# Kernel optimization log

Measured on AMD Instinct MI355X. Metric: run time of the kernel, lower is better.

## Reference

```python
import jax, jax.numpy as jnp
import numpy as np

NUM_ELEM = 62
DEGREE = 3
M = 64  # matrix_size = sqrt(layer_sizes[0]) = sqrt(4096)
IN_DIM, H = 4096, 2048
N_POINTS = 2_097_152


def _glorot(k, shape):
    lim = np.float32(np.sqrt(2.0 / (shape[0] + shape[1])))
    return jax.random.normal(k, shape, jnp.float32) * lim


def setup_inputs() -> dict:
    key = jax.random.key(0)
    ks = jax.random.split(key, 4)
    points = jax.random.uniform(ks[0], (N_POINTS, 2), jnp.float32)
    # first coordinate lives in [-1, 1) (original maps it via (x+1)/2)
    points = points.at[:, 0].set(points[:, 0] * 2.0 - 1.0)
    return {
        "points": points,
        "W1": _glorot(ks[1], (IN_DIM, H)), "b1": jnp.zeros((H,), jnp.float32),
        "W2": _glorot(ks[2], (H, H)),      "b2": jnp.zeros((H,), jnp.float32),
        "W3": _glorot(ks[3], (H, 1)),      "b3": jnp.zeros((1,), jnp.float32),
    }


def _quadratic(t):
    # tfg bspline._quadratic: 3 quadratic B-spline basis functions of t in [0,1)
    return jnp.stack([(1.0 - t) ** 2 * 0.5, -t * t + t + 0.5, t * t * 0.5], axis=-1)


def _spline(coord):
    p = coord * NUM_ELEM
    pos = jnp.minimum(jnp.floor(p).astype(jnp.int32) + 1, NUM_ELEM)  # tf.cond clamp
    return _quadratic(jnp.mod(p, 1.0)), pos


def reference(points, W1, b1, W2, b2, W3, b3):
    # cofs = eye(4096); identity @ W1 == W1, so the first Dense reduces to W1 + b1
    h = jnp.tanh(W1 + b1)
    h = jnp.tanh(h @ W2 + b2)
    out = jnp.tanh(h @ W3 + b3)          # [4096, 1]
    u = out.reshape(M, M) * 3.0           # control-point grid [64, 64]

    x = (points[:, 0] + 1.0) * 0.5
    y = points[:, 1]
    bx, px = _spline(x)                   # bx: [N,3], px: [N]
    by, py = _spline(y)
    offs = jnp.arange(DEGREE)
    ix = px[:, None] - 1 + offs           # [N,3] row indices into u
    iy = py[:, None] - 1 + offs           # [N,3] col indices into u
    Wn = u[ix[:, :, None], iy[:, None, :]]  # [N,3,3] local control-point windows
    # sum_{i,j} W[i,j] * splines_x[i] * splines_y[j]  (meshgrid orientation)
    return jnp.einsum('nij,ni,nj->n', Wn, bx, by)
```

## Files before the change

### kernel.cpp

```cpp
#include <hip/hip_runtime.h>
#include <stdint.h>

#define IN_DIM 4096
#define H_DIM  2048
#define NPTS   2097152

typedef short  bf16x8  __attribute__((ext_vector_type(8)));
typedef float  floatx4 __attribute__((ext_vector_type(4)));

__device__ __forceinline__ unsigned short f2bf(float f) {
    unsigned u = __float_as_uint(f);
    unsigned r = (u + 0x7FFFu + ((u >> 16) & 1u)) >> 16;
    return (unsigned short)r;
}

__global__ void prep_h(const float* __restrict__ W1, const float* __restrict__ b1,
                       unsigned short* __restrict__ hbf, float* __restrict__ rowsum) {
    if (blockIdx.x < 16) rowsum[blockIdx.x * 256 + threadIdx.x] = 0.0f;
    int idx = (blockIdx.x * 256 + threadIdx.x) * 4;
    float4 w = *(const float4*)(W1 + idx);
    float4 b = *(const float4*)(b1 + (idx & (H_DIM - 1)));
    ushort4 o;
    o.x = f2bf(tanhf(w.x + b.x));
    o.y = f2bf(tanhf(w.y + b.y));
    o.z = f2bf(tanhf(w.z + b.z));
    o.w = f2bf(tanhf(w.w + b.w));
    *(ushort4*)(hbf + idx) = o;
}

__global__ void prep_w2t(const float* __restrict__ W2, unsigned short* __restrict__ W2T) {
    __shared__ unsigned short tile[64][66];
    int k0 = blockIdx.y * 64, n0 = blockIdx.x * 64;
    for (int idx = threadIdx.x; idx < 64 * 64; idx += 256) {
        int r = idx >> 6, c = idx & 63;
        tile[c][r] = f2bf(W2[(size_t)(k0 + r) * H_DIM + n0 + c]);
    }
    __syncthreads();
    for (int idx = threadIdx.x; idx < 64 * 64; idx += 256) {
        int r = idx >> 6, c = idx & 63;
        W2T[(size_t)(n0 + r) * H_DIM + k0 + c] = tile[r][c];
    }
}

#define BK 32
__global__ __launch_bounds__(256, 4) void gemm_fused(
    const unsigned short* __restrict__ A,
    const unsigned short* __restrict__ BT,
    const float* __restrict__ b2, const float* __restrict__ W3,
    float* __restrict__ rowsum) {
    __shared__ __align__(16) unsigned short As[128 * BK];
    __shared__ __align__(16) unsigned short Bs[64 * BK];
    const int K = H_DIM;
    const int t = threadIdx.x;
    const int w = t >> 6, l = t & 63;
    const int lane16 = l & 15, quad = l >> 4;
    const int wr = w >> 1, wc = w & 1;
    const int rowBase = blockIdx.y * 128;
    const int colBase = blockIdx.x * 64;

    const unsigned short* aSrc = A  + (size_t)(rowBase + (t >> 2)) * K + (t & 3) * 8;
    const unsigned short* bSrc = BT + (size_t)(colBase + (t >> 2)) * K + (t & 3) * 8;
    unsigned short* aDst = As + (w << 9);
    unsigned short* bDst = Bs + (w << 9);

    floatx4 acc[4][2];
    floatx4 zero = {0.f, 0.f, 0.f, 0.f};
#pragma unroll
    for (int i = 0; i < 4; ++i)
#pragma unroll
        for (int j = 0; j < 2; ++j) acc[i][j] = zero;

    for (int k0 = 0; k0 < K; k0 += BK) {
        __syncthreads();
        __builtin_amdgcn_global_load_lds(
            (const __attribute__((address_space(1))) void*)(aSrc + k0),
            (__attribute__((address_space(3))) void*)aDst, 16, 0, 0);
        __builtin_amdgcn_global_load_lds(
            (const __attribute__((address_space(1))) void*)(aSrc + (size_t)64 * K + k0),
            (__attribute__((address_space(3))) void*)(aDst + 2048), 16, 0, 0);
        __builtin_amdgcn_global_load_lds(
            (const __attribute__((address_space(1))) void*)(bSrc + k0),
            (__attribute__((address_space(3))) void*)bDst, 16, 0, 0);
        __syncthreads();

        bf16x8 af[4], bfr[2];
#pragma unroll
        for (int mi = 0; mi < 4; ++mi)
            af[mi] = *(const bf16x8*)(As + (wr * 64 + mi * 16 + lane16) * BK + quad * 8);
#pragma unroll
        for (int ni = 0; ni < 2; ++ni)
            bfr[ni] = *(const bf16x8*)(Bs + (wc * 32 + ni * 16 + lane16) * BK + quad * 8);
#pragma unroll
        for (int mi = 0; mi < 4; ++mi)
#pragma unroll
            for (int ni = 0; ni < 2; ++ni)
                acc[mi][ni] = __builtin_amdgcn_mfma_f32_16x16x32_bf16(
                    af[mi], bfr[ni], acc[mi][ni], 0, 0, 0);
    }

    const int rowG = rowBase + wr * 64;
#pragma unroll
    for (int mi = 0; mi < 4; ++mi) {
#pragma unroll
        for (int r = 0; r < 4; ++r) {
            float s = 0.f;
#pragma unroll
            for (int ni = 0; ni < 2; ++ni) {
                int col = colBase + wc * 32 + ni * 16 + lane16;
                float v = acc[mi][ni][r] + b2[col];
                s += tanhf(v) * W3[col];
            }
#pragma unroll
            for (int off = 1; off < 16; off <<= 1) s += __shfl_xor(s, off, 64);
            if (lane16 == 0)
                atomicAdd(&rowsum[rowG + mi * 16 + quad * 4 + r], s);
        }
    }
}

__global__ void spline_kernel(const float2* __restrict__ pts,
                              const float* __restrict__ rowsum,
                              const float* __restrict__ b3,
                              float* __restrict__ out, int n) {
    __shared__ float us[4096];
    float bias = b3[0];
    for (int i = threadIdx.x; i < 4096; i += blockDim.x)
        us[i] = 3.0f * tanhf(rowsum[i] + bias);
    __syncthreads();
    int stride = gridDim.x * blockDim.x;
    for (int idx = blockIdx.x * blockDim.x + threadIdx.x; idx < n; idx += stride) {
        float2 pt = pts[idx];
        float x = (pt.x + 1.0f) * 0.5f;
        float y = pt.y;
        float px = x * 62.0f, py = y * 62.0f;
        float fx = floorf(px), fy = floorf(py);
        int posx = min((int)fx + 1, 62);
        int posy = min((int)fy + 1, 62);
        float tx = px - fx, ty = py - fy;
        float bx0 = 0.5f * (1.f - tx) * (1.f - tx);
        float bx1 = -tx * tx + tx + 0.5f;
        float bx2 = 0.5f * tx * tx;
        float by0 = 0.5f * (1.f - ty) * (1.f - ty);
        float by1 = -ty * ty + ty + 0.5f;
        float by2 = 0.5f * ty * ty;
        int ix = posx - 1, iy = posy - 1;
        const float* r0 = &us[ix * 64 + iy];
        const float* r1 = r0 + 64;
        const float* r2 = r1 + 64;
        float s0 = r0[0] * by0 + r0[1] * by1 + r0[2] * by2;
        float s1 = r1[0] * by0 + r1[1] * by1 + r1[2] * by2;
        float s2 = r2[0] * by0 + r2[1] * by1 + r2[2] * by2;
        out[idx] = bx0 * s0 + bx1 * s1 + bx2 * s2;
    }
}

extern "C" void kernel_launch(void* const* d_in, const int* in_sizes, int n_in,
                              void* d_out, int out_size, void* d_ws, size_t ws_size,
                              hipStream_t stream) {
    const float* points = (const float*)d_in[0];
    const float* W1 = (const float*)d_in[1];
    const float* b1 = (const float*)d_in[2];
    const float* W2 = (const float*)d_in[3];
    const float* b2 = (const float*)d_in[4];
    const float* W3 = (const float*)d_in[5];
    const float* b3 = (const float*)d_in[6];
    float* out = (float*)d_out;

    char* ws = (char*)d_ws;
    unsigned short* hbf = (unsigned short*)ws;
    unsigned short* w2t = (unsigned short*)(ws + 16777216);
    float* rowsum = (float*)(ws + 25165824);

    prep_h<<<8192, 256, 0, stream>>>(W1, b1, hbf, rowsum);
    prep_w2t<<<dim3(32, 32), 256, 0, stream>>>(W2, w2t);
    gemm_fused<<<dim3(H_DIM / 64, IN_DIM / 128), 256, 0, stream>>>(hbf, w2t, b2, W3, rowsum);
    spline_kernel<<<1024, 256, 0, stream>>>((const float2*)points, rowsum, b3, out, NPTS);
}
```

Baseline: 181.9 us.

## Double-buffer GEMM LDS tiles, merge prep kernels, vectorize spline loads

The GEMM now double-buffers its A/B LDS tiles, issuing global_load_lds for the next K-slice before computing the current one and dropping one barrier per iteration. The LDS layout is reorganised so each wave loads 16-row fragments laid out to match the MFMA read pattern. The two prep kernels are merged into one launch, and the spline kernel handles two points per thread with float4 loads and float2 stores. The aim is to overlap global latency with MFMA work and cut launch and memory-transaction overhead. The cost is doubled LDS use, and correctness depends on there being no wait for the async LDS loads before the single barrier.

```diff
diff --git a/kernel.cpp b/kernel.cpp
--- a/kernel.cpp
+++ b/kernel.cpp
@@ -14,31 +14,35 @@
     return (unsigned short)r;
 }
 
-__global__ void prep_h(const float* __restrict__ W1, const float* __restrict__ b1,
-                       unsigned short* __restrict__ hbf, float* __restrict__ rowsum) {
-    if (blockIdx.x < 16) rowsum[blockIdx.x * 256 + threadIdx.x] = 0.0f;
-    int idx = (blockIdx.x * 256 + threadIdx.x) * 4;
-    float4 w = *(const float4*)(W1 + idx);
-    float4 b = *(const float4*)(b1 + (idx & (H_DIM - 1)));
-    ushort4 o;
-    o.x = f2bf(tanhf(w.x + b.x));
-    o.y = f2bf(tanhf(w.y + b.y));
-    o.z = f2bf(tanhf(w.z + b.z));
-    o.w = f2bf(tanhf(w.w + b.w));
-    *(ushort4*)(hbf + idx) = o;
-}
-
-__global__ void prep_w2t(const float* __restrict__ W2, unsigned short* __restrict__ W2T) {
+__global__ void prep_all(const float* __restrict__ W1, const float* __restrict__ b1,
+                         const float* __restrict__ W2,
+                         unsigned short* __restrict__ hbf, unsigned short* __restrict__ W2T,
+                         float* __restrict__ rowsum) {
     __shared__ unsigned short tile[64][66];
-    int k0 = blockIdx.y * 64, n0 = blockIdx.x * 64;
-    for (int idx = threadIdx.x; idx < 64 * 64; idx += 256) {
-        int r = idx >> 6, c = idx & 63;
-        tile[c][r] = f2bf(W2[(size_t)(k0 + r) * H_DIM + n0 + c]);
-    }
-    __syncthreads();
-    for (int idx = threadIdx.x; idx < 64 * 64; idx += 256) {
-        int r = idx >> 6, c = idx & 63;
-        W2T[(size_t)(n0 + r) * H_DIM + k0 + c] = tile[r][c];
+    int b = blockIdx.x;
+    if (b < 8192) {
+        if (b < 16) rowsum[b * 256 + threadIdx.x] = 0.0f;
+        int idx = (b * 256 + threadIdx.x) * 4;
+        float4 w = *(const float4*)(W1 + idx);
+        float4 bb = *(const float4*)(b1 + (idx & (H_DIM - 1)));
+        ushort4 o;
+        o.x = f2bf(tanhf(w.x + bb.x));
+        o.y = f2bf(tanhf(w.y + bb.y));
+        o.z = f2bf(tanhf(w.z + bb.z));
+        o.w = f2bf(tanhf(w.w + bb.w));
+        *(ushort4*)(hbf + idx) = o;
+    } else {
+        int bb = b - 8192;
+        int k0 = (bb >> 5) * 64, n0 = (bb & 31) * 64;
+        for (int idx = threadIdx.x; idx < 64 * 64; idx += 256) {
+            int r = idx >> 6, c = idx & 63;
+            tile[c][r] = f2bf(W2[(size_t)(k0 + r) * H_DIM + n0 + c]);
+        }
+        __syncthreads();
+        for (int idx = threadIdx.x; idx < 64 * 64; idx += 256) {
+            int r = idx >> 6, c = idx & 63;
+            W2T[(size_t)(n0 + r) * H_DIM + k0 + c] = tile[r][c];
+        }
     }
 }
 
@@ -48,8 +52,8 @@
     const unsigned short* __restrict__ BT,
     const float* __restrict__ b2, const float* __restrict__ W3,
     float* __restrict__ rowsum) {
-    __shared__ __align__(16) unsigned short As[128 * BK];
-    __shared__ __align__(16) unsigned short Bs[64 * BK];
+    __shared__ __align__(16) unsigned short As[2][128 * BK];
+    __shared__ __align__(16) unsigned short Bs[2][64 * BK];
     const int K = H_DIM;
     const int t = threadIdx.x;
     const int w = t >> 6, l = t & 63;
@@ -58,10 +62,9 @@
     const int rowBase = blockIdx.y * 128;
     const int colBase = blockIdx.x * 64;
 
-    const unsigned short* aSrc = A  + (size_t)(rowBase + (t >> 2)) * K + (t & 3) * 8;
-    const unsigned short* bSrc = BT + (size_t)(colBase + (t >> 2)) * K + (t & 3) * 8;
-    unsigned short* aDst = As + (w << 9);
-    unsigned short* bDst = Bs + (w << 9);
+    const unsigned short* aSrc0 = A + (size_t)(rowBase + w * 16 + lane16) * K + quad * 8;
+    const unsigned short* aSrc1 = aSrc0 + (size_t)64 * K;
+    const unsigned short* bSrc  = BT + (size_t)(colBase + w * 16 + lane16) * K + quad * 8;
 
     floatx4 acc[4][2];
     floatx4 zero = {0.f, 0.f, 0.f, 0.f};
@@ -70,32 +73,46 @@
 #pragma unroll
         for (int j = 0; j < 2; ++j) acc[i][j] = zero;
 
+    __builtin_amdgcn_global_load_lds(
+        (const __attribute__((address_space(1))) void*)(aSrc0),
+        (__attribute__((address_space(3))) void*)(&As[0][w * 512]), 16, 0, 0);
+    __builtin_amdgcn_global_load_lds(
+        (const __attribute__((address_space(1))) void*)(aSrc1),
+        (__attribute__((address_space(3))) void*)(&As[0][(w + 4) * 512]), 16, 0, 0);
+    __builtin_amdgcn_global_load_lds(
+        (const __attribute__((address_space(1))) void*)(bSrc),
+        (__attribute__((address_space(3))) void*)(&Bs[0][w * 512]), 16, 0, 0);
+
+    int buf = 0;
     for (int k0 = 0; k0 < K; k0 += BK) {
         __syncthreads();
-        __builtin_amdgcn_global_load_lds(
-            (const __attribute__((address_space(1))) void*)(aSrc + k0),
-            (__attribute__((address_space(3))) void*)aDst, 16, 0, 0);
-        __builtin_amdgcn_global_load_lds(
-            (const __attribute__((address_space(1))) void*)(aSrc + (size_t)64 * K + k0),
-            (__attribute__((address_space(3))) void*)(aDst + 2048), 16, 0, 0);
-        __builtin_amdgcn_global_load_lds(
-            (const __attribute__((address_space(1))) void*)(bSrc + k0),
-            (__attribute__((address_space(3))) void*)bDst, 16, 0, 0);
-        __syncthreads();
+        if (k0 + BK < K) {
+            int nb = buf ^ 1;
+            __builtin_amdgcn_global_load_lds(
+                (const __attribute__((address_space(1))) void*)(aSrc0 + k0 + BK),
+                (__attribute__((address_space(3))) void*)(&As[nb][w * 512]), 16, 0, 0);
+            __builtin_amdgcn_global_load_lds(
+                (const __attribute__((address_space(1))) void*)(aSrc1 + k0 + BK),
+                (__attribute__((address_space(3))) void*)(&As[nb][(w + 4) * 512]), 16, 0, 0);
+            __builtin_amdgcn_global_load_lds(
+                (const __attribute__((address_space(1))) void*)(bSrc + k0 + BK),
+                (__attribute__((address_space(3))) void*)(&Bs[nb][w * 512]), 16, 0, 0);
+        }
 
         bf16x8 af[4], bfr[2];
 #pragma unroll
         for (int mi = 0; mi < 4; ++mi)
-            af[mi] = *(const bf16x8*)(As + (wr * 64 + mi * 16 + lane16) * BK + quad * 8);
+            af[mi] = *(const bf16x8*)(&As[buf][(wr * 4 + mi) * 512 + quad * 128 + lane16 * 8]);
 #pragma unroll
         for (int ni = 0; ni < 2; ++ni)
-            bfr[ni] = *(const bf16x8*)(Bs + (wc * 32 + ni * 16 + lane16) * BK + quad * 8);
+            bfr[ni] = *(const bf16x8*)(&Bs[buf][(wc * 2 + ni) * 512 + quad * 128 + lane16 * 8]);
 #pragma unroll
         for (int mi = 0; mi < 4; ++mi)
 #pragma unroll
             for (int ni = 0; ni < 2; ++ni)
                 acc[mi][ni] = __builtin_amdgcn_mfma_f32_16x16x32_bf16(
                     af[mi], bfr[ni], acc[mi][ni], 0, 0, 0);
+        buf ^= 1;
     }
 
     const int rowG = rowBase + wr * 64;
@@ -118,39 +135,44 @@
     }
 }
 
-__global__ void spline_kernel(const float2* __restrict__ pts,
+__device__ __forceinline__ float spline_eval(const float* us, float ptx, float pty) {
+    float x = (ptx + 1.0f) * 0.5f;
+    float px = x * 62.0f, py = pty * 62.0f;
+    float fx = floorf(px), fy = floorf(py);
+    int posx = min((int)fx + 1, 62);
+    int posy = min((int)fy + 1, 62);
+    float tx = px - fx, ty = py - fy;
+    float bx0 = 0.5f * (1.f - tx) * (1.f - tx);
+    float bx1 = -tx * tx + tx + 0.5f;
+    float bx2 = 0.5f * tx * tx;
+    float by0 = 0.5f * (1.f - ty) * (1.f - ty);
+    float by1 = -ty * ty + ty + 0.5f;
+    float by2 = 0.5f * ty * ty;
+    const float* r0 = &us[(posx - 1) * 64 + (posy - 1)];
+    const float* r1 = r0 + 64;
+    const float* r2 = r1 + 64;
+    float s0 = r0[0] * by0 + r0[1] * by1 + r0[2] * by2;
+    float s1 = r1[0] * by0 + r1[1] * by1 + r1[2] * by2;
+    float s2 = r2[0] * by0 + r2[1] * by1 + r2[2] * by2;
+    return bx0 * s0 + bx1 * s1 + bx2 * s2;
+}
+
+__global__ void spline_kernel(const float4* __restrict__ pts,
                               const float* __restrict__ rowsum,
                               const float* __restrict__ b3,
-                              float* __restrict__ out, int n) {
+                              float2* __restrict__ out, int npairs) {
     __shared__ float us[4096];
     float bias = b3[0];
     for (int i = threadIdx.x; i < 4096; i += blockDim.x)
         us[i] = 3.0f * tanhf(rowsum[i] + bias);
     __syncthreads();
     int stride = gridDim.x * blockDim.x;
-    for (int idx = blockIdx.x * blockDim.x + threadIdx.x; idx < n; idx += stride) {
-        float2 pt = pts[idx];
-        float x = (pt.x + 1.0f) * 0.5f;
-        float y = pt.y;
-        float px = x * 62.0f, py = y * 62.0f;
-        float fx = floorf(px), fy = floorf(py);
-        int posx = min((int)fx + 1, 62);
-        int posy = min((int)fy + 1, 62);
-        float tx = px - fx, ty = py - fy;
-        float bx0 = 0.5f * (1.f - tx) * (1.f - tx);
-        float bx1 = -tx * tx + tx + 0.5f;
-        float bx2 = 0.5f * tx * tx;
-        float by0 = 0.5f * (1.f - ty) * (1.f - ty);
-        float by1 = -ty * ty + ty + 0.5f;
-        float by2 = 0.5f * ty * ty;
-        int ix = posx - 1, iy = posy - 1;
-        const float* r0 = &us[ix * 64 + iy];
-        const float* r1 = r0 + 64;
-        const float* r2 = r1 + 64;
-        float s0 = r0[0] * by0 + r0[1] * by1 + r0[2] * by2;
-        float s1 = r1[0] * by0 + r1[1] * by1 + r1[2] * by2;
-        float s2 = r2[0] * by0 + r2[1] * by1 + r2[2] * by2;
-        out[idx] = bx0 * s0 + bx1 * s1 + bx2 * s2;
+    for (int idx = blockIdx.x * blockDim.x + threadIdx.x; idx < npairs; idx += stride) {
+        float4 p2 = pts[idx];
+        float2 o;
+        o.x = spline_eval(us, p2.x, p2.y);
+        o.y = spline_eval(us, p2.z, p2.w);
+        out[idx] = o;
     }
 }
 
@@ -171,8 +193,8 @@
     unsigned short* w2t = (unsigned short*)(ws + 16777216);
     float* rowsum = (float*)(ws + 25165824);
 
-    prep_h<<<8192, 256, 0, stream>>>(W1, b1, hbf, rowsum);
-    prep_w2t<<<dim3(32, 32), 256, 0, stream>>>(W2, w2t);
+    prep_all<<<8192 + 1024, 256, 0, stream>>>(W1, b1, W2, hbf, w2t, rowsum);
     gemm_fused<<<dim3(H_DIM / 64, IN_DIM / 128), 256, 0, stream>>>(hbf, w2t, b2, W3, rowsum);
-    spline_kernel<<<1024, 256, 0, stream>>>((const float2*)points, rowsum, b3, out, NPTS);
-}
+    spline_kernel<<<1024, 256, 0, stream>>>((const float4*)points, rowsum, b3,
+                                            (float2*)out, NPTS / 2);
+}
```

Result: slower. 213.4 us (+17.3%).
